# Kernel tuning notes

Measured on AMD Instinct MI355X. Metric: run time of the kernel, lower is better.

Reference implementation:

```python
import jax, jax.numpy as jnp
import numpy as np

B, H, S, D = 4, 16, 2048, 64

def setup_inputs() -> dict:
    key = jax.random.key(0)
    kq, kk, kv = jax.random.split(key, 3)
    q = jax.random.normal(kq, (B, H, S, D), dtype=jnp.float32)
    k = jax.random.normal(kk, (B, H, S, D), dtype=jnp.float32)
    v = jax.random.normal(kv, (B, H, S, D), dtype=jnp.float32)
    mask = jnp.zeros((B, 1, 1, S), dtype=jnp.float32)  # additive mask
    return {"q": q, "k": k, "v": v, "mask": mask}

def reference(q, k, v, mask):
    dk = q.shape[-1]
    scale = 1.0 / np.sqrt(dk).astype(np.float32)
    # [B,H,S,S] attention logits
    scores = jnp.einsum('bhqd,bhkd->bhqk', q, k) * scale
    scores = scores + mask  # broadcast additive mask
    attention = jax.nn.softmax(scores, axis=-1)
    # dropout p=0.0 -> identity
    context = jnp.einsum('bhqk,bhkd->bhqd', attention, v)
    return (context, attention)
```

## Files before the change

### kernel.cpp

```cpp
#include <hip/hip_runtime.h>

namespace {
constexpr int kB = 4, kH = 16, kS = 2048, kD = 64;
constexpr int ROWS = 64;
constexpr int KT = 64;
constexpr int NT = kS / KT;
constexpr float SCALE = 0.125f;
constexpr long long CTXN = (long long)kB * kH * kS * kD;
}

typedef __attribute__((ext_vector_type(4))) float f32x4;
typedef __attribute__((ext_vector_type(8))) short bf16x8;

__device__ __forceinline__ short f2bf(float f) {
  union { float f; unsigned u; } x; x.f = f;
  return (short)((x.u + 0x7fffu + ((x.u >> 16) & 1u)) >> 16);
}

__device__ __forceinline__ f32x4 mfma16(bf16x8 a, bf16x8 b, f32x4 c) {
  return __builtin_amdgcn_mfma_f32_16x16x32_bf16(a, b, c, 0, 0, 0);
}

__device__ __forceinline__ void cvt_row16(short* dst, const float4* src) {
  float4 f0 = src[0], f1 = src[1], f2 = src[2], f3 = src[3];
  bf16x8 h0, h1;
  h0[0] = f2bf(f0.x); h0[1] = f2bf(f0.y); h0[2] = f2bf(f0.z); h0[3] = f2bf(f0.w);
  h0[4] = f2bf(f1.x); h0[5] = f2bf(f1.y); h0[6] = f2bf(f1.z); h0[7] = f2bf(f1.w);
  h1[0] = f2bf(f2.x); h1[1] = f2bf(f2.y); h1[2] = f2bf(f2.z); h1[3] = f2bf(f2.w);
  h1[4] = f2bf(f3.x); h1[5] = f2bf(f3.y); h1[6] = f2bf(f3.z); h1[7] = f2bf(f3.w);
  *(bf16x8*)(dst) = h0;
  *(bf16x8*)(dst + 8) = h1;
}

__global__ __launch_bounds__(256, 3)
void attn_fwd(const float* __restrict__ q, const float* __restrict__ kk,
              const float* __restrict__ vv, const float* __restrict__ mask,
              float* __restrict__ outctx, float* __restrict__ outatt) {
  __shared__ short q_s[ROWS][72];
  __shared__ short k_s[KT][72];
  __shared__ short vt_s[kD][72];
  __shared__ short p_s[4][16][72];
  __shared__ float mask_s[kS];

  const int tid = threadIdx.x;
  const int lane = tid & 63;
  const int wave = tid >> 6;
  const int quad = lane >> 4;
  const int l16 = lane & 15;

  const int bh = blockIdx.x >> 5;
  const int qt = blockIdx.x & 31;
  const int qbase = qt * ROWS;
  const int bb = bh >> 4;

  const float* qg = q + ((size_t)bh * kS + qbase) * kD;
  const float* kg = kk + (size_t)bh * kS * kD;
  const float* vg = vv + (size_t)bh * kS * kD;
  const float* mg = mask + (size_t)bb * kS;

  for (int i = tid; i < kS / 4; i += 256)
    ((float4*)mask_s)[i] = ((const float4*)mg)[i];

  {
    const int row = tid >> 2, c0 = (tid & 3) << 4;
    cvt_row16(&q_s[row][c0], (const float4*)(qg + row * kD + c0));
  }
  __syncthreads();

  const bf16x8 a0 = *(const bf16x8*)&q_s[wave * 16 + l16][quad * 8];
  const bf16x8 a1 = *(const bf16x8*)&q_s[wave * 16 + l16][32 + quad * 8];

  float rs[4] = {0.f, 0.f, 0.f, 0.f};
  for (int t = 0; t < NT; ++t) {
    __syncthreads();
    {
      const int row = tid >> 2, c0 = (tid & 3) << 4;
      cvt_row16(&k_s[row][c0],
                (const float4*)(kg + ((size_t)(t * KT + row)) * kD + c0));
    }
    __syncthreads();
#pragma unroll
    for (int ct = 0; ct < 4; ++ct) {
      const bf16x8 b0 = *(const bf16x8*)&k_s[ct * 16 + l16][quad * 8];
      const bf16x8 b1 = *(const bf16x8*)&k_s[ct * 16 + l16][32 + quad * 8];
      f32x4 acc = {0.f, 0.f, 0.f, 0.f};
      acc = mfma16(a0, b0, acc);
      acc = mfma16(a1, b1, acc);
      const float mk = mask_s[t * KT + ct * 16 + l16];
#pragma unroll
      for (int r = 0; r < 4; ++r)
        rs[r] += __expf(acc[r] * SCALE + mk);
    }
  }

  float rcl[4];
#pragma unroll
  for (int r = 0; r < 4; ++r) {
    float s = rs[r];
    s += __shfl_xor(s, 1);
    s += __shfl_xor(s, 2);
    s += __shfl_xor(s, 4);
    s += __shfl_xor(s, 8);
    rcl[r] = 1.0f / s;
  }

  f32x4 o[4];
#pragma unroll
  for (int dt = 0; dt < 4; ++dt) o[dt] = (f32x4){0.f, 0.f, 0.f, 0.f};

  float* attw = outatt + ((size_t)bh * kS + qbase + wave * 16 + quad * 4) * kS;

  for (int t = 0; t < NT; ++t) {
    __syncthreads();
    {
      const int row = tid >> 2, c0 = (tid & 3) << 4;
      cvt_row16(&k_s[row][c0],
                (const float4*)(kg + ((size_t)(t * KT + row)) * kD + c0));
      const float4* vsrc = (const float4*)(vg + ((size_t)(t * KT + row)) * kD + c0);
      float4 g0 = vsrc[0], g1 = vsrc[1], g2 = vsrc[2], g3 = vsrc[3];
      vt_s[c0 + 0][row] = f2bf(g0.x);  vt_s[c0 + 1][row] = f2bf(g0.y);
      vt_s[c0 + 2][row] = f2bf(g0.z);  vt_s[c0 + 3][row] = f2bf(g0.w);
      vt_s[c0 + 4][row] = f2bf(g1.x);  vt_s[c0 + 5][row] = f2bf(g1.y);
      vt_s[c0 + 6][row] = f2bf(g1.z);  vt_s[c0 + 7][row] = f2bf(g1.w);
      vt_s[c0 + 8][row] = f2bf(g2.x);  vt_s[c0 + 9][row] = f2bf(g2.y);
      vt_s[c0 + 10][row] = f2bf(g2.z); vt_s[c0 + 11][row] = f2bf(g2.w);
      vt_s[c0 + 12][row] = f2bf(g3.x); vt_s[c0 + 13][row] = f2bf(g3.y);
      vt_s[c0 + 14][row] = f2bf(g3.z); vt_s[c0 + 15][row] = f2bf(g3.w);
    }
    __syncthreads();
#pragma unroll
    for (int ct = 0; ct < 4; ++ct) {
      const bf16x8 b0 = *(const bf16x8*)&k_s[ct * 16 + l16][quad * 8];
      const bf16x8 b1 = *(const bf16x8*)&k_s[ct * 16 + l16][32 + quad * 8];
      f32x4 acc = {0.f, 0.f, 0.f, 0.f};
      acc = mfma16(a0, b0, acc);
      acc = mfma16(a1, b1, acc);
      const float mk = mask_s[t * KT + ct * 16 + l16];
      const int col = t * KT + ct * 16 + l16;
#pragma unroll
      for (int r = 0; r < 4; ++r) {
        const float p = __expf(acc[r] * SCALE + mk) * rcl[r];
        attw[(size_t)r * kS + col] = p;
        p_s[wave][quad * 4 + r][ct * 16 + l16] = f2bf(p);
      }
    }
    __builtin_amdgcn_wave_barrier();
    const bf16x8 pa0 = *(const bf16x8*)&p_s[wave][l16][quad * 8];
    const bf16x8 pa1 = *(const bf16x8*)&p_s[wave][l16][32 + quad * 8];
#pragma unroll
    for (int dt = 0; dt < 4; ++dt) {
      const bf16x8 w0 = *(const bf16x8*)&vt_s[dt * 16 + l16][quad * 8];
      const bf16x8 w1 = *(const bf16x8*)&vt_s[dt * 16 + l16][32 + quad * 8];
      o[dt] = mfma16(pa0, w0, o[dt]);
      o[dt] = mfma16(pa1, w1, o[dt]);
    }
  }

  float* cw = outctx + ((size_t)bh * kS + qbase + wave * 16 + quad * 4) * kD;
#pragma unroll
  for (int dt = 0; dt < 4; ++dt)
#pragma unroll
    for (int r = 0; r < 4; ++r)
      cw[(size_t)r * kD + dt * 16 + l16] = o[dt][r];
}

extern "C" void kernel_launch(void* const* d_in, const int* in_sizes, int n_in,
                              void* d_out, int out_size, void* d_ws, size_t ws_size,
                              hipStream_t stream) {
  const float* q = (const float*)d_in[0];
  const float* k = (const float*)d_in[1];
  const float* v = (const float*)d_in[2];
  const float* mask = (const float*)d_in[3];
  float* ctx = (float*)d_out;
  float* att = (float*)d_out + CTXN;
  attn_fwd<<<dim3(kB * kH * NT), dim3(256), 0, stream>>>(q, k, v, mask, ctx, att);
}
```

Baseline: 1.423 ms.

## Pre-convert Q/K/V to swizzled bf16 and stream tiles via async global-to-LDS loads

Adds two pre-pass kernels that convert Q and K to bf16 and V to a transposed bf16 layout in workspace, all with an XOR swizzle, so the attention kernel no longer converts fp32 per tile. The main kernel loads tiles with global_load_lds directly into LDS, double-buffers K and V across iterations with manual vmcnt waits and barriers, and raises priority around the PV MFMAs. The aim is to cut the redundant fp32 reads and conversions repeated by each query block, and to overlap loads with compute. In exchange it adds extra launches and workspace traffic, and relies on fragile hand-counted waitcnt synchronisation. It falls back to the old kernel when no workspace is given.

```diff
diff --git a/kernel.cpp b/kernel.cpp
--- a/kernel.cpp
+++ b/kernel.cpp
@@ -7,6 +7,8 @@
 constexpr int NT = kS / KT;
 constexpr float SCALE = 0.125f;
 constexpr long long CTXN = (long long)kB * kH * kS * kD;
+constexpr size_t TENS = (size_t)kB * kH * kS * kD;
+constexpr size_t WS_NEED = TENS * sizeof(short) * 3;
 }
 
 typedef __attribute__((ext_vector_type(4))) float f32x4;
@@ -19,6 +21,199 @@
 
 __device__ __forceinline__ f32x4 mfma16(bf16x8 a, bf16x8 b, f32x4 c) {
   return __builtin_amdgcn_mfma_f32_16x16x32_bf16(a, b, c, 0, 0, 0);
+}
+
+__device__ __forceinline__ void gload16(const void* g, void* l) {
+  __builtin_amdgcn_global_load_lds(
+      (const __attribute__((address_space(1))) unsigned*)g,
+      (__attribute__((address_space(3))) unsigned*)l, 16, 0, 0);
+}
+
+__device__ __forceinline__ bf16x8 frag_ld(const short* base, int row, int chunk) {
+  return *(const bf16x8*)(base + row * 64 + ((chunk ^ (row & 7)) << 3));
+}
+
+__device__ __forceinline__ void stage_rows(short* dst, const short* src,
+                                           int wave, int lane) {
+  gload16(src + wave * 1024 + lane * 8, dst + wave * 1024);
+  gload16(src + wave * 1024 + 512 + lane * 8, dst + wave * 1024 + 512);
+}
+
+__device__ __forceinline__ void stage_vt(short* dst, const short* vg, int t,
+                                         int wave, int lane) {
+  const int d0 = wave * 16 + (lane >> 3);
+  gload16(vg + (size_t)d0 * kS + t * 64 + (lane & 7) * 8, dst + wave * 1024);
+  gload16(vg + (size_t)(d0 + 8) * kS + t * 64 + (lane & 7) * 8,
+          dst + wave * 1024 + 512);
+}
+
+__global__ __launch_bounds__(256)
+void convert_qk(const float* __restrict__ q, const float* __restrict__ k,
+                short* __restrict__ qb, short* __restrict__ kb) {
+  const unsigned idx = blockIdx.x * 256 + threadIdx.x;
+  const unsigned i = idx & 0xFFFFFu;
+  const bool isk = (idx >> 20) != 0;
+  const unsigned row = i >> 3, c = i & 7;
+  const float* src = (isk ? k : q) + ((size_t)row << 6) + (c << 3);
+  short* dst = (isk ? kb : qb) + ((size_t)row << 6) + ((c ^ (row & 7u)) << 3);
+  const float4 f0 = ((const float4*)src)[0];
+  const float4 f1 = ((const float4*)src)[1];
+  bf16x8 h;
+  h[0] = f2bf(f0.x); h[1] = f2bf(f0.y); h[2] = f2bf(f0.z); h[3] = f2bf(f0.w);
+  h[4] = f2bf(f1.x); h[5] = f2bf(f1.y); h[6] = f2bf(f1.z); h[7] = f2bf(f1.w);
+  *(bf16x8*)dst = h;
+}
+
+__global__ __launch_bounds__(256)
+void convert_vt(const float* __restrict__ v, short* __restrict__ vtb) {
+  const int gw = blockIdx.x * 4 + (threadIdx.x >> 6);
+  const int d = threadIdx.x & 63;
+  const int bh = gw >> 8;
+  const int so = (gw & 255) << 3;
+  const float* src = v + ((size_t)bh * kS + so) * kD + d;
+  bf16x8 h;
+#pragma unroll
+  for (int i = 0; i < 8; ++i) h[i] = f2bf(src[(size_t)i * kD]);
+  short* dst = vtb + (size_t)bh * kS * kD + (size_t)d * kS + (so & ~63)
+             + ((((so >> 3) & 7) ^ (d & 7)) << 3);
+  *(bf16x8*)dst = h;
+}
+
+__global__ __launch_bounds__(256, 3)
+void attn_fast(const short* __restrict__ qb, const short* __restrict__ kb,
+               const short* __restrict__ vtb, const float* __restrict__ mask,
+               float* __restrict__ outctx, float* __restrict__ outatt) {
+  __shared__ short q_s[64 * 64];
+  __shared__ short k_s[64 * 64];
+  __shared__ short v_s[2][64 * 64];
+  __shared__ short p_s[4][16][72];
+  __shared__ float mask_s[kS];
+
+  const int tid = threadIdx.x;
+  const int lane = tid & 63;
+  const int wave = tid >> 6;
+  const int quad = lane >> 4;
+  const int l16 = lane & 15;
+
+  const int bh = blockIdx.x >> 5;
+  const int qt = blockIdx.x & 31;
+  const int qbase = qt * ROWS;
+  const int bb = bh >> 4;
+
+  const short* qgp = qb + ((size_t)bh * kS + qbase) * kD;
+  const short* kgp = kb + (size_t)bh * kS * kD;
+  const short* vgp = vtb + (size_t)bh * kS * kD;
+  const float* mg = mask + (size_t)bb * kS;
+
+  for (int i = tid; i < kS / 4; i += 256)
+    ((float4*)mask_s)[i] = ((const float4*)mg)[i];
+
+  stage_rows(q_s, qgp, wave, lane);
+  stage_rows(k_s, kgp, wave, lane);
+  __syncthreads();
+
+  const int arow = wave * 16 + l16;
+  const bf16x8 a0 = frag_ld(q_s, arow, quad);
+  const bf16x8 a1 = frag_ld(q_s, arow, 4 + quad);
+
+  float rs[4] = {0.f, 0.f, 0.f, 0.f};
+#pragma unroll 1
+  for (int t = 0; t < NT; ++t) {
+    const short* cur = (t & 1) ? v_s[0] : k_s;
+    if (t + 1 < NT)
+      stage_rows((t & 1) ? k_s : v_s[0], kgp + ((size_t)(t + 1) << 12), wave, lane);
+#pragma unroll
+    for (int ct = 0; ct < 4; ++ct) {
+      const int row = ct * 16 + l16;
+      const bf16x8 b0 = frag_ld(cur, row, quad);
+      const bf16x8 b1 = frag_ld(cur, row, 4 + quad);
+      f32x4 acc = {0.f, 0.f, 0.f, 0.f};
+      acc = mfma16(a0, b0, acc);
+      acc = mfma16(a1, b1, acc);
+      const float mk = mask_s[t * KT + ct * 16 + l16];
+#pragma unroll
+      for (int r = 0; r < 4; ++r)
+        rs[r] += __expf(acc[r] * SCALE + mk);
+    }
+    __syncthreads();
+  }
+
+  float rcl[4];
+#pragma unroll
+  for (int r = 0; r < 4; ++r) {
+    float s = rs[r];
+    s += __shfl_xor(s, 1);
+    s += __shfl_xor(s, 2);
+    s += __shfl_xor(s, 4);
+    s += __shfl_xor(s, 8);
+    rcl[r] = 1.0f / s;
+  }
+
+  f32x4 o[4];
+#pragma unroll
+  for (int dt = 0; dt < 4; ++dt) o[dt] = (f32x4){0.f, 0.f, 0.f, 0.f};
+
+  float* attw = outatt + ((size_t)bh * kS + qbase + wave * 16 + quad * 4) * kS;
+
+  stage_rows(k_s, kgp, wave, lane);
+  stage_vt(v_s[0], vgp, 0, wave, lane);
+  __syncthreads();
+
+#pragma unroll 1
+  for (int t = 0; t < NT; ++t) {
+#pragma unroll
+    for (int ct = 0; ct < 4; ++ct) {
+      const int row = ct * 16 + l16;
+      const bf16x8 b0 = frag_ld(k_s, row, quad);
+      const bf16x8 b1 = frag_ld(k_s, row, 4 + quad);
+      f32x4 acc = {0.f, 0.f, 0.f, 0.f};
+      acc = mfma16(a0, b0, acc);
+      acc = mfma16(a1, b1, acc);
+      const float mk = mask_s[t * KT + ct * 16 + l16];
+      const int col = t * KT + ct * 16 + l16;
+#pragma unroll
+      for (int r = 0; r < 4; ++r) {
+        const float p = __expf(acc[r] * SCALE + mk) * rcl[r];
+        attw[(size_t)r * kS + col] = p;
+        p_s[wave][quad * 4 + r][ct * 16 + l16] = f2bf(p);
+      }
+    }
+    __builtin_amdgcn_wave_barrier();
+    const bf16x8 pa0 = *(const bf16x8*)&p_s[wave][l16][quad * 8];
+    const bf16x8 pa1 = *(const bf16x8*)&p_s[wave][l16][32 + quad * 8];
+
+    asm volatile("s_waitcnt vmcnt(16)" ::: "memory");
+    __builtin_amdgcn_s_barrier();
+    asm volatile("" ::: "memory");
+
+    if (t + 1 < NT) {
+      stage_rows(k_s, kgp + ((size_t)(t + 1) << 12), wave, lane);
+      stage_vt(v_s[(t + 1) & 1], vgp, t + 1, wave, lane);
+    }
+
+    const short* vt = v_s[t & 1];
+    __builtin_amdgcn_s_setprio(1);
+#pragma unroll
+    for (int dt = 0; dt < 4; ++dt) {
+      const int row = dt * 16 + l16;
+      const bf16x8 w0 = frag_ld(vt, row, quad);
+      const bf16x8 w1 = frag_ld(vt, row, 4 + quad);
+      o[dt] = mfma16(pa0, w0, o[dt]);
+      o[dt] = mfma16(pa1, w1, o[dt]);
+    }
+    __builtin_amdgcn_s_setprio(0);
+
+    asm volatile("s_waitcnt vmcnt(2)" ::: "memory");
+    __builtin_amdgcn_s_barrier();
+    asm volatile("" ::: "memory");
+  }
+
+  float* cw = outctx + ((size_t)bh * kS + qbase + wave * 16 + quad * 4) * kD;
+#pragma unroll
+  for (int dt = 0; dt < 4; ++dt)
+#pragma unroll
+    for (int r = 0; r < 4; ++r)
+      cw[(size_t)r * kD + dt * 16 + l16] = o[dt][r];
 }
 
 __device__ __forceinline__ void cvt_row16(short* dst, const float4* src) {
@@ -173,5 +368,16 @@
   const float* mask = (const float*)d_in[3];
   float* ctx = (float*)d_out;
   float* att = (float*)d_out + CTXN;
-  attn_fwd<<<dim3(kB * kH * NT), dim3(256), 0, stream>>>(q, k, v, mask, ctx, att);
-}
+  if (d_ws != nullptr && ws_size >= WS_NEED) {
+    short* qb = (short*)d_ws;
+    short* kb = qb + TENS;
+    short* vtb = kb + TENS;
+    convert_qk<<<dim3(8192), dim3(256), 0, stream>>>(q, k, qb, kb);
+    convert_vt<<<dim3(4096), dim3(256), 0, stream>>>(v, vtb);
+    attn_fast<<<dim3(kB * kH * NT), dim3(256), 0, stream>>>(qb, kb, vtb, mask,
+                                                            ctx, att);
+  } else {
+    attn_fwd<<<dim3(kB * kH * NT), dim3(256), 0, stream>>>(q, k, v, mask, ctx,
+                                                           att);
+  }
+}
```

Result: faster. 1.383 ms (-2.8%).
